# Performance work log

Measured on AMD Instinct MI355X. Metric: run time of the kernel, lower is better.

## Reference

```python
import jax, jax.numpy as jnp
import numpy as np

B, F_BINS, K = 8192, 2048, 6
LS, LBW, BWMAX = 0.1, 0.05, 4.0   # lambda_sparse, lambda_bw_excess, bw_soft_max
LAP, LPK, LUM = 0.5, 0.3, 0.1     # lambda_ap, lambda_peaks, lambda_unmatched
BIG = 1e9


def _huber_mean(p, t):
    # F.huber_loss with delta=1.0, mean reduction
    e = p - t
    a = jnp.abs(e)
    return jnp.mean(jnp.where(a < 1.0, 0.5 * e * e, a - 0.5))


def _soft_match_peaks(pred_cfs, gt_cfs, gt_mask):
    """Greedy nearest-neighbour matching, sequential over the K GT slots."""
    b, k = pred_cfs.shape
    dist = jnp.abs(gt_cfs[:, :, None] - pred_cfs[:, None, :])  # [B, K_gt, K_pred]
    active = gt_mask > 0.5                                      # [B, K]

    def step(slot_used, inp):
        d_j, act_j = inp                               # [B, K], [B]
        d_m = jnp.where(slot_used, BIG, d_j)
        best = jnp.argmin(d_m, axis=1)                 # [B]
        idx = jnp.where(act_j, best, -1)
        hit = (best[:, None] == jnp.arange(k)[None, :]) & act_j[:, None]
        return slot_used | hit, idx

    used0 = jnp.zeros((b, k), dtype=bool)
    used, match_idx = jax.lax.scan(step, used0, (jnp.moveaxis(dist, 1, 0), active.T))
    matched = used.astype(pred_cfs.dtype)
    return match_idx.T, matched, 1.0 - matched  # [B,K] long, [B,K] float, [B,K] float


def _total_loss(pred_psd, true_psd, cfs, amps, bws, exponent, offset,
                gt_cfs, gt_amps, gt_bws, gt_offset, gt_exponent, peak_mask):
    # reconstruction terms
    l_recon = _huber_mean(pred_psd, true_psd)
    l_sparse = jnp.mean(amps)
    bw_excess = jnp.maximum(bws - BWMAX, 0.0)
    l_bw = jnp.mean(bw_excess * bw_excess)
    total = l_recon + LS * l_sparse + LBW * l_bw

    # supervised aperiodic term
    l_ap = jnp.mean((exponent[:, 0] - gt_exponent) ** 2) + jnp.mean((offset[:, 0] - gt_offset) ** 2)

    # matched peak terms
    match_idx, matched, unmatched = _soft_match_peaks(cfs, gt_cfs, peak_mask)
    n_real = jnp.maximum(jnp.sum(peak_mask), 1.0)
    idx = jnp.maximum(match_idx, 0)
    # torch leaves GT columns with no active entry at zero
    col_any = jnp.any(peak_mask > 0.5, axis=0)

    def gathered(v):
        return jnp.where(col_any[None, :], jnp.take_along_axis(v, idx, axis=1), 0.0)

    def masked_mse(p, t):
        return jnp.sum(((p - t) ** 2) * peak_mask) / n_real

    l_peaks = (masked_mse(gathered(cfs), gt_cfs)
               + masked_mse(gathered(amps), gt_amps)
               + masked_mse(gathered(bws), gt_bws))
    l_um = jnp.sum(amps * unmatched) / jnp.maximum(jnp.sum(unmatched), 1.0)

    return total + LAP * l_ap + LPK * l_peaks + LUM * l_um


def setup_inputs() -> dict:
    key = jax.random.key(0)
    ks = jax.random.split(key, 13)
    peak_mask = jax.random.randint(ks[7], (B, K), 0, 2).astype(jnp.float32)
    return {
        "pred_psd": jax.random.normal(ks[0], (B, F_BINS), dtype=jnp.float32),
        "true_psd": jax.random.normal(ks[1], (B, F_BINS), dtype=jnp.float32),
        "cfs": jax.random.uniform(ks[2], (B, K), minval=1.0, maxval=30.0),
        "amps": jax.random.uniform(ks[3], (B, K), minval=0.0, maxval=1.5),
        "bws": jax.random.uniform(ks[4], (B, K), minval=0.5, maxval=6.0),
        "exponent": jax.random.normal(ks[5], (B, 1), dtype=jnp.float32),
        "offset": jax.random.normal(ks[6], (B, 1), dtype=jnp.float32),
        # GT peaks: sorted ascending, zero-padded where mask==0
        "gt_cfs": jnp.sort(jax.random.uniform(ks[8], (B, K), minval=1.0, maxval=30.0), axis=1) * peak_mask,
        "gt_amps": jax.random.uniform(ks[9], (B, K), minval=0.0, maxval=1.5) * peak_mask,
        "gt_bws": jax.random.uniform(ks[10], (B, K), minval=0.5, maxval=6.0) * peak_mask,
        "gt_offset": jax.random.normal(ks[11], (B,), dtype=jnp.float32),
        "gt_exponent": jax.random.normal(ks[12], (B,), dtype=jnp.float32),
        "peak_mask": peak_mask,
    }


def reference(pred_psd, true_psd, cfs, amps, bws, exponent, offset,
              gt_cfs, gt_amps, gt_bws, gt_offset, gt_exponent, peak_mask):
    return _total_loss(pred_psd, true_psd, cfs, amps, bws, exponent, offset,
                       gt_cfs, gt_amps, gt_bws, gt_offset, gt_exponent, peak_mask)
```

## Files before the change

### kernel.cpp

```cpp
#include <hip/hip_runtime.h>

#define BATCH   8192
#define FBINS   2048
#define KSLOTS  6

#define HTHREADS 512
#define HWAVES   (HTHREADS / 64)
#define HBLOCKS  2048
#define BLK_F4   2048
#define WAVE_F4  (BLK_F4 / HWAVES)
#define SPT      4

#define RBLOCKS   (BATCH / HTHREADS)
#define TOTBLOCKS (HBLOCKS + RBLOCKS)

#define LS   0.1f
#define LBW  0.05f
#define BWMAX 4.0f
#define LAP  0.5f
#define LPK  0.3f
#define LUM  0.1f

__device__ __forceinline__ void gload16(const void* g, void* l) {
    __builtin_amdgcn_global_load_lds(
        (const __attribute__((address_space(1))) void*)g,
        (__attribute__((address_space(3))) void*)l, 16, 0, 0);
}

__device__ __forceinline__ float huber4(float4 a, float4 b) {
    float s = 0.f;
    { float e = a.x - b.x; float ab = fabsf(e); s += (ab < 1.f) ? 0.5f * e * e : ab - 0.5f; }
    { float e = a.y - b.y; float ab = fabsf(e); s += (ab < 1.f) ? 0.5f * e * e : ab - 0.5f; }
    { float e = a.z - b.z; float ab = fabsf(e); s += (ab < 1.f) ? 0.5f * e * e : ab - 0.5f; }
    { float e = a.w - b.w; float ab = fabsf(e); s += (ab < 1.f) ? 0.5f * e * e : ab - 0.5f; }
    return s;
}

__global__ __launch_bounds__(HTHREADS) void fused_partial(
    const float* __restrict__ pred,  const float* __restrict__ tgt,
    const float* __restrict__ cfs,   const float* __restrict__ amps,
    const float* __restrict__ bws,   const float* __restrict__ expn,
    const float* __restrict__ offs,  const float* __restrict__ gt_cfs,
    const float* __restrict__ gt_amps, const float* __restrict__ gt_bws,
    const float* __restrict__ gt_off, const float* __restrict__ gt_exp,
    const float* __restrict__ mask,
    float* __restrict__ hpart, float* __restrict__ rpart)
{
    __shared__ float4 ldsA[BLK_F4];
    __shared__ float4 ldsB[BLK_F4];
    __shared__ float  wred[HWAVES][8];

    const int tid  = threadIdx.x;
    const int wave = tid >> 6;
    const int lane = tid & 63;

    if (blockIdx.x < HBLOCKS) {
        const float4* __restrict__ a4 = (const float4*)pred;
        const float4* __restrict__ b4 = (const float4*)tgt;
        const int wbase = wave * WAVE_F4;
        const long long gbase = (long long)blockIdx.x * BLK_F4 + wbase;

        #pragma unroll
        for (int s = 0; s < SPT; s++)
            gload16(&a4[gbase + s * 64 + lane], &ldsA[wbase + s * 64]);
        #pragma unroll
        for (int s = 0; s < SPT; s++)
            gload16(&b4[gbase + s * 64 + lane], &ldsB[wbase + s * 64]);
        asm volatile("s_waitcnt vmcnt(0)" ::: "memory");

        float ssum = 0.f;
        #pragma unroll
        for (int s = 0; s < SPT; s++) {
            float4 a = ldsA[wbase + s * 64 + lane];
            float4 b = ldsB[wbase + s * 64 + lane];
            ssum += huber4(a, b);
        }

        #pragma unroll
        for (int o = 32; o > 0; o >>= 1)
            ssum += __shfl_down(ssum, o, 64);
        if (lane == 0) wred[wave][0] = ssum;
        __syncthreads();
        if (tid == 0) {
            float t = 0.f;
            #pragma unroll
            for (int w = 0; w < HWAVES; w++) t += wred[w][0];
            hpart[blockIdx.x] = t;
        }
        return;
    }

    const int rb = blockIdx.x - HBLOCKS;
    const int b = rb * HTHREADS + tid;

    float acc[7];
    #pragma unroll
    for (int c = 0; c < 7; c++) acc[c] = 0.f;

    {
        float c[KSLOTS], a[KSLOTS], w[KSLOTS];
        float gc[KSLOTS], ga[KSLOTS], gw[KSLOTS], m[KSLOTS];
        #pragma unroll
        for (int i = 0; i < KSLOTS; i++) {
            c[i]  = cfs[b * KSLOTS + i];
            a[i]  = amps[b * KSLOTS + i];
            w[i]  = bws[b * KSLOTS + i];
            gc[i] = gt_cfs[b * KSLOTS + i];
            ga[i] = gt_amps[b * KSLOTS + i];
            gw[i] = gt_bws[b * KSLOTS + i];
            m[i]  = mask[b * KSLOTS + i];
        }

        bool used[KSLOTS];
        #pragma unroll
        for (int i = 0; i < KSLOTS; i++) used[i] = false;

        for (int j = 0; j < KSLOTS; j++) {
            if (m[j] > 0.5f) {
                int best = -1;
                float bd = 3.402823e+38f;
                #pragma unroll
                for (int i = 0; i < KSLOTS; i++) {
                    if (!used[i]) {
                        float d = fabsf(gc[j] - c[i]);
                        if (d < bd) { bd = d; best = i; }
                    }
                }
                used[best] = true;
                float dc = c[best] - gc[j];
                float da = a[best] - ga[j];
                float dw = w[best] - gw[j];
                acc[3] += dc * dc + da * da + dw * dw;
                acc[4] += 1.f;
            }
        }

        #pragma unroll
        for (int i = 0; i < KSLOTS; i++) {
            acc[0] += a[i];
            float ex = fmaxf(w[i] - BWMAX, 0.f);
            acc[1] += ex * ex;
            if (!used[i]) { acc[5] += 1.f; acc[6] += a[i]; }
        }

        float de = expn[b] - gt_exp[b];
        float dof = offs[b] - gt_off[b];
        acc[2] = de * de + dof * dof;
    }

    #pragma unroll
    for (int c = 0; c < 7; c++) {
        float v = acc[c];
        #pragma unroll
        for (int o = 32; o > 0; o >>= 1)
            v += __shfl_down(v, o, 64);
        acc[c] = v;
    }
    if (lane == 0) {
        #pragma unroll
        for (int c = 0; c < 7; c++) wred[wave][c] = acc[c];
    }
    __syncthreads();
    if (tid < 7) {
        float t = 0.f;
        #pragma unroll
        for (int w = 0; w < HWAVES; w++) t += wred[w][tid];
        rpart[7 * rb + tid] = t;
    }
}

__global__ __launch_bounds__(256) void finalize(
    const float* __restrict__ hpart, const float* __restrict__ rpart,
    float* __restrict__ out)
{
    __shared__ double sm[256];
    double s = 0.0;
    #pragma unroll
    for (int r = 0; r < HBLOCKS / 256; r++)
        s += (double)hpart[r * 256 + threadIdx.x];
    sm[threadIdx.x] = s;
    __syncthreads();
    for (int o = 128; o > 0; o >>= 1) {
        if (threadIdx.x < o) sm[threadIdx.x] += sm[threadIdx.x + o];
        __syncthreads();
    }

    if (threadIdx.x == 0) {
        double huber_total = sm[0];
        double acc[7];
        for (int c = 0; c < 7; c++) acc[c] = 0.0;
        for (int blk = 0; blk < RBLOCKS; blk++)
            for (int c = 0; c < 7; c++)
                acc[c] += (double)rpart[7 * blk + c];

        double l_recon  = huber_total / ((double)BATCH * FBINS);
        double l_sparse = acc[0] / ((double)BATCH * KSLOTS);
        double l_bw     = acc[1] / ((double)BATCH * KSLOTS);
        double l_ap     = acc[2] / (double)BATCH;
        double n_real   = acc[4] > 1.0 ? acc[4] : 1.0;
        double l_peaks  = acc[3] / n_real;
        double n_um     = acc[5] > 1.0 ? acc[5] : 1.0;
        double l_um     = acc[6] / n_um;

        double total = l_recon + (double)LS * l_sparse + (double)LBW * l_bw
                     + (double)LAP * l_ap + (double)LPK * l_peaks + (double)LUM * l_um;
        out[0] = (float)total;
    }
}

extern "C" void kernel_launch(void* const* d_in, const int* in_sizes, int n_in,
                              void* d_out, int out_size, void* d_ws, size_t ws_size,
                              hipStream_t stream) {
    const float* pred_psd = (const float*)d_in[0];
    const float* true_psd = (const float*)d_in[1];
    const float* cfs      = (const float*)d_in[2];
    const float* amps     = (const float*)d_in[3];
    const float* bws      = (const float*)d_in[4];
    const float* expn     = (const float*)d_in[5];
    const float* offs     = (const float*)d_in[6];
    const float* gt_cfs   = (const float*)d_in[7];
    const float* gt_amps  = (const float*)d_in[8];
    const float* gt_bws   = (const float*)d_in[9];
    const float* gt_off   = (const float*)d_in[10];
    const float* gt_exp   = (const float*)d_in[11];
    const float* mask     = (const float*)d_in[12];
    float* out = (float*)d_out;

    float* hpart = (float*)d_ws;
    float* rpart = hpart + HBLOCKS;

    fused_partial<<<TOTBLOCKS, HTHREADS, 0, stream>>>(
        pred_psd, true_psd, cfs, amps, bws, expn, offs,
        gt_cfs, gt_amps, gt_bws, gt_off, gt_exp, mask, hpart, rpart);
    finalize<<<1, 256, 0, stream>>>(hpart, rpart, out);
}
```

Measured before the change: 30.98 us.

## Double-buffer LDS tiles in persistent huber blocks to overlap loads with compute

```diff
diff --git a/kernel.cpp b/kernel.cpp
--- a/kernel.cpp
+++ b/kernel.cpp
@@ -5,11 +5,12 @@
 #define KSLOTS  6
 
 #define HTHREADS 512
-#define HWAVES   (HTHREADS / 64)
-#define HBLOCKS  2048
-#define BLK_F4   2048
-#define WAVE_F4  (BLK_F4 / HWAVES)
-#define SPT      4
+#define HWAVES   8
+#define HBLOCKS  512
+#define TILES    8
+#define TILE_F4  1024
+#define WTILE_F4 (TILE_F4 / HWAVES)
+#define BLK_F4   (TILES * TILE_F4)
 
 #define RBLOCKS   (BATCH / HTHREADS)
 #define TOTBLOCKS (HBLOCKS + RBLOCKS)
@@ -21,7 +22,7 @@
 #define LPK  0.3f
 #define LUM  0.1f
 
-__device__ __forceinline__ void gload16(const void* g, void* l) {
+__device__ __forceinline__ void gload16(const float4* g, float4* l) {
     __builtin_amdgcn_global_load_lds(
         (const __attribute__((address_space(1))) void*)g,
         (__attribute__((address_space(3))) void*)l, 16, 0, 0);
@@ -46,8 +47,8 @@
     const float* __restrict__ mask,
     float* __restrict__ hpart, float* __restrict__ rpart)
 {
-    __shared__ float4 ldsA[BLK_F4];
-    __shared__ float4 ldsB[BLK_F4];
+    __shared__ float4 ldsA[2][TILE_F4];
+    __shared__ float4 ldsB[2][TILE_F4];
     __shared__ float  wred[HWAVES][8];
 
     const int tid  = threadIdx.x;
@@ -57,23 +58,41 @@
     if (blockIdx.x < HBLOCKS) {
         const float4* __restrict__ a4 = (const float4*)pred;
         const float4* __restrict__ b4 = (const float4*)tgt;
-        const int wbase = wave * WAVE_F4;
-        const long long gbase = (long long)blockIdx.x * BLK_F4 + wbase;
-
-        #pragma unroll
-        for (int s = 0; s < SPT; s++)
-            gload16(&a4[gbase + s * 64 + lane], &ldsA[wbase + s * 64]);
-        #pragma unroll
-        for (int s = 0; s < SPT; s++)
-            gload16(&b4[gbase + s * 64 + lane], &ldsB[wbase + s * 64]);
-        asm volatile("s_waitcnt vmcnt(0)" ::: "memory");
+        const int woff  = wave * WTILE_F4;
+        const int gbase = blockIdx.x * BLK_F4 + woff + lane;
+
+        {
+            const float4* ga = a4 + gbase;
+            const float4* gb = b4 + gbase;
+            gload16(ga,      &ldsA[0][woff]);
+            gload16(ga + 64, &ldsA[0][woff + 64]);
+            gload16(gb,      &ldsB[0][woff]);
+            gload16(gb + 64, &ldsB[0][woff + 64]);
+        }
 
         float ssum = 0.f;
         #pragma unroll
-        for (int s = 0; s < SPT; s++) {
-            float4 a = ldsA[wbase + s * 64 + lane];
-            float4 b = ldsB[wbase + s * 64 + lane];
-            ssum += huber4(a, b);
+        for (int t = 0; t < TILES; t++) {
+            const int buf = t & 1;
+            if (t + 1 < TILES) {
+                const float4* ga = a4 + gbase + (t + 1) * TILE_F4;
+                const float4* gb = b4 + gbase + (t + 1) * TILE_F4;
+                gload16(ga,      &ldsA[buf ^ 1][woff]);
+                gload16(ga + 64, &ldsA[buf ^ 1][woff + 64]);
+                gload16(gb,      &ldsB[buf ^ 1][woff]);
+                gload16(gb + 64, &ldsB[buf ^ 1][woff + 64]);
+                asm volatile("s_waitcnt vmcnt(4)" ::: "memory");
+            } else {
+                asm volatile("s_waitcnt vmcnt(0)" ::: "memory");
+            }
+            __builtin_amdgcn_sched_barrier(0);
+
+            float4 a0 = ldsA[buf][woff + lane];
+            float4 b0 = ldsB[buf][woff + lane];
+            float4 a1 = ldsA[buf][woff + 64 + lane];
+            float4 b1 = ldsB[buf][woff + 64 + lane];
+            ssum += huber4(a0, b0);
+            ssum += huber4(a1, b1);
         }
 
         #pragma unroll
```

After: 30.75 us. Within noise of the previous version (-0.7%).
